# Optimization experiments

Hardware: AMD Instinct MI355X
Metric: run time of the kernel (lower is better)

Reference implementation:

```python
import jax, jax.numpy as jnp
import numpy as np
from jax.scipy.special import logsumexp

B, N, T, D = 32, 400, 315, 512   # batch, fMRI parcels, text/task rows, feature dim
H = 256
EPS = 1e-5                       # InstanceNorm2d default eps
N_ITERS = 100                    # sinkhorn_rpm n_iters


def setup_inputs() -> dict:
    key = jax.random.key(0)
    ks = jax.random.split(key, 6)
    features = jax.random.normal(ks[0], (B, N, D), jnp.float32)
    text = jax.random.normal(ks[1], (T, D), jnp.float32)
    # Affinity bilinear weight, init near identity as in graph-matching Affinity modules
    A = jnp.eye(D, dtype=jnp.float32) + 0.01 * jax.random.normal(ks[2], (D, D), jnp.float32)
    gamma = jnp.ones((), jnp.float32)   # InstanceNorm2d(1, affine=True) weight
    beta = jnp.zeros((), jnp.float32)   # InstanceNorm2d(1, affine=True) bias
    Wh = jax.random.normal(ks[3], (2 * D, H), jnp.float32) / np.float32(np.sqrt(2 * D))
    bh = jnp.zeros((H,), jnp.float32)
    Wo = jax.random.normal(ks[4], (H, 1), jnp.float32) / np.float32(np.sqrt(H))
    bo = jnp.zeros((1,), jnp.float32)
    return {"features": features, "text": text, "A": A, "gamma": gamma,
            "beta": beta, "Wh": Wh, "bh": bh, "Wo": Wo, "bo": bo}


def _forward(features, text, A, gamma, beta, Wh, bh, Wo, bo):
    # Affinity: s[b,n,t] = features[b,n,:] @ A @ text[t,:]   -> [B, N, T]
    s = jnp.einsum('bnd,de,te->bnt', features, A, text)
    # InstanceNorm2d(1, affine): normalize each [N,T] map per batch element (single channel)
    m = jnp.mean(s, axis=(1, 2), keepdims=True)
    v = jnp.var(s, axis=(1, 2), keepdims=True)
    s = gamma * (s - m) * jax.lax.rsqrt(v + EPS) + beta
    # sinkhorn_rpm: log-domain alternating row/col normalization, no slack
    def body(log_a, _):
        log_a = log_a - logsumexp(log_a, axis=2, keepdims=True)  # row normalization
        log_a = log_a - logsumexp(log_a, axis=1, keepdims=True)  # col normalization
        return log_a, None
    log_s, _ = jax.lax.scan(body, s, None, length=N_ITERS)
    s1 = jnp.exp(log_s)                                   # [B, N, T]
    # features_t @ s1, then transpose -> [B, T, D]
    features1 = jnp.einsum('bnd,bnt->btd', features, s1)
    text1 = jnp.broadcast_to(text[None], (features.shape[0], T, D))
    combine = jnp.concatenate([features1, text1], axis=2)  # [B, T, 2D]
    h = jax.nn.relu(combine @ Wh + bh)                     # [B, T, H]
    pred = (h @ Wo + bo)[..., 0]                           # [B, T] == [B, num_tasks]
    return pred


def reference(features, text, A, gamma, beta, Wh, bh, Wo, bo):
    return _forward(features, text, A, gamma, beta, Wh, bh, Wo, bo)
```

## Files before the change

kernel.cpp:

```cpp
#include <hip/hip_runtime.h>
#include <hip/hip_fp16.h>

#define BDIM 32
#define NDIM 400
#define TDIM 315
#define TPAD 320
#define DDIM 512
#define HDIM 256
#define NITER 100

#define OFS_TAB   0u
#define OFS_TB    327680u
#define OFS_STATS 655360u
#define OFS_WHB   655616u
#define OFS_S     1048576u
#define OFS_S1B   9240576u
#define OFS_F1    17432576u
#define OFS_FB    27754496u
#define OFS_QPART (OFS_F1 + 4096u)

typedef __attribute__((ext_vector_type(8))) short bf16x8;
typedef __attribute__((ext_vector_type(4))) float f32x4;
typedef unsigned long long ull;

__device__ __forceinline__ unsigned rne_hi(float x) {
  unsigned u = __float_as_uint(x);
  u += 0x7fffu + ((u >> 16) & 1u);
  return u & 0xffff0000u;
}
__device__ __forceinline__ unsigned pack2(float lo, float hi) {
  return (rne_hi(lo) >> 16) | rne_hi(hi);
}
__device__ __forceinline__ unsigned short bf1(float x) { return (unsigned short)(rne_hi(x) >> 16); }
__device__ __forceinline__ float bfres(float x) {
  return x - __uint_as_float(rne_hi(x));
}

template <int CTRL, int RMASK>
__device__ __forceinline__ float dppadd(float x) {
  int y = __builtin_amdgcn_update_dpp(0, __float_as_int(x), CTRL, RMASK, 0xf, true);
  return x + __int_as_float(y);
}
template <int CTRL, int RMASK>
__device__ __forceinline__ float dppmax(float x) {
  int y = __builtin_amdgcn_update_dpp(0, __float_as_int(x), CTRL, RMASK, 0xf, true);
  return fmaxf(x, __int_as_float(y));
}

#define LDH 40

__global__ __launch_bounds__(256) void k_prep(const float* __restrict__ F,
                                              const float* __restrict__ Wh,
                                              const float* __restrict__ text,
                                              const float* __restrict__ A,
                                              const float* __restrict__ bh,
                                              unsigned short* __restrict__ Fb,
                                              unsigned short* __restrict__ Whb,
                                              unsigned short* __restrict__ tAb,
                                              float* __restrict__ TB,
                                              float* __restrict__ stats,
                                              uint4* __restrict__ qzero) {
  __shared__ unsigned short Ahs[64 * LDH], Als[64 * LDH];
  __shared__ unsigned short Bhs[64 * LDH], Bls[64 * LDH];
  const int bid = blockIdx.x, tid = threadIdx.x;
  if (bid >= 60) {
    const int NF4 = (BDIM * NDIM * DDIM) / 4;
    const int NW4 = (DDIM * HDIM) / 4;
    const int NQ4 = (2 * BDIM * 8 * 320 * 2) / 4;
    const int gid = (bid - 60) * 256 + tid;
    const int stride = 452 * 256;
    for (int i = gid; i < NF4; i += stride) {
      float4 v = ((const float4*)F)[i];
      ((uint2*)Fb)[i] = make_uint2(pack2(v.x, v.y), pack2(v.z, v.w));
    }
    for (int i = gid; i < NW4; i += stride) {
      float4 v = ((const float4*)Wh)[i];
      ((uint2*)Whb)[i] = make_uint2(pack2(v.x, v.y), pack2(v.z, v.w));
    }
    for (int i = gid; i < NQ4; i += stride) qzero[i] = make_uint4(0u, 0u, 0u, 0u);
    if (gid < BDIM * 2) stats[gid] = 0.0f;
    return;
  }
  const int l = tid & 63, wv = tid >> 6;
  const int m = tid >> 2, kq = (tid & 3) * 8;
  f32x4 acc[4] = {};
  if (bid < 40) {
    const int d0 = (bid & 7) * 64, t0 = (bid >> 3) * 64;
    for (int k0 = 0; k0 < 512; k0 += 32) {
      {
        int t = t0 + m;
        float4 v0 = make_float4(0.f, 0.f, 0.f, 0.f), v1 = v0;
        if (t < TDIM) {
          v0 = *(const float4*)(text + (size_t)t * DDIM + k0 + kq);
          v1 = *(const float4*)(text + (size_t)t * DDIM + k0 + kq + 4);
        }
        *(uint4*)(&Ahs[m * LDH + kq]) =
            make_uint4(pack2(v0.x, v0.y), pack2(v0.z, v0.w), pack2(v1.x, v1.y), pack2(v1.z, v1.w));
        *(uint4*)(&Als[m * LDH + kq]) =
            make_uint4(pack2(bfres(v0.x), bfres(v0.y)), pack2(bfres(v0.z), bfres(v0.w)),
                       pack2(bfres(v1.x), bfres(v1.y)), pack2(bfres(v1.z), bfres(v1.w)));
        float4 w0 = *(const float4*)(A + (size_t)(d0 + m) * DDIM + k0 + kq);
        float4 w1 = *(const float4*)(A + (size_t)(d0 + m) * DDIM + k0 + kq + 4);
        *(uint4*)(&Bhs[m * LDH + kq]) =
            make_uint4(pack2(w0.x, w0.y), pack2(w0.z, w0.w), pack2(w1.x, w1.y), pack2(w1.z, w1.w));
        *(uint4*)(&Bls[m * LDH + kq]) =
            make_uint4(pack2(bfres(w0.x), bfres(w0.y)), pack2(bfres(w0.z), bfres(w0.w)),
                       pack2(bfres(w1.x), bfres(w1.y)), pack2(bfres(w1.z), bfres(w1.w)));
      }
      __syncthreads();
      bf16x8 ah = *(const bf16x8*)(&Ahs[(wv * 16 + (l & 15)) * LDH + (l >> 4) * 8]);
      bf16x8 al = *(const bf16x8*)(&Als[(wv * 16 + (l & 15)) * LDH + (l >> 4) * 8]);
#pragma unroll
      for (int c = 0; c < 4; ++c) {
        bf16x8 bh_ = *(const bf16x8*)(&Bhs[(c * 16 + (l & 15)) * LDH + (l >> 4) * 8]);
        bf16x8 bl_ = *(const bf16x8*)(&Bls[(c * 16 + (l & 15)) * LDH + (l >> 4) * 8]);
        acc[c] = __builtin_amdgcn_mfma_f32_16x16x32_bf16(ah, bh_, acc[c], 0, 0, 0);
        acc[c] = __builtin_amdgcn_mfma_f32_16x16x32_bf16(ah, bl_, acc[c], 0, 0, 0);
        acc[c] = __builtin_amdgcn_mfma_f32_16x16x32_bf16(al, bh_, acc[c], 0, 0, 0);
      }
      __syncthreads();
    }
#pragma unroll
    for (int c = 0; c < 4; ++c)
#pragma unroll
      for (int r = 0; r < 4; ++r) {
        int t = t0 + wv * 16 + ((l >> 4) << 2) + r;
        int d = d0 + c * 16 + (l & 15);
        tAb[(size_t)t * DDIM + d] = bf1(acc[c][r]);
      }
  } else {
    const int idx = bid - 40;
    const int h0 = (idx & 3) * 64, t0 = (idx >> 2) * 64;
    const float* Wb = Wh + DDIM * HDIM;
    const int col = tid & 31, g = tid >> 5;
    for (int k0 = 0; k0 < 512; k0 += 32) {
      {
        int t = t0 + m;
        float4 v0 = make_float4(0.f, 0.f, 0.f, 0.f), v1 = v0;
        if (t < TDIM) {
          v0 = *(const float4*)(text + (size_t)t * DDIM + k0 + kq);
          v1 = *(const float4*)(text + (size_t)t * DDIM + k0 + kq + 4);
        }
        *(uint4*)(&Ahs[m * LDH + kq]) =
            make_uint4(pack2(v0.x, v0.y), pack2(v0.z, v0.w), pack2(v1.x, v1.y), pack2(v1.z, v1.w));
        *(uint4*)(&Als[m * LDH + kq]) =
            make_uint4(pack2(bfres(v0.x), bfres(v0.y)), pack2(bfres(v0.z), bfres(v0.w)),
                       pack2(bfres(v1.x), bfres(v1.y)), pack2(bfres(v1.z), bfres(v1.w)));
        float4 w0 = *(const float4*)(Wb + (size_t)(k0 + col) * HDIM + h0 + g * 8);
        float4 w1 = *(const float4*)(Wb + (size_t)(k0 + col) * HDIM + h0 + g * 8 + 4);
        float wr[8] = {w0.x, w0.y, w0.z, w0.w, w1.x, w1.y, w1.z, w1.w};
#pragma unroll
        for (int i = 0; i < 8; ++i) {
          Bhs[(g * 8 + i) * LDH + col] = bf1(wr[i]);
          Bls[(g * 8 + i) * LDH + col] = bf1(bfres(wr[i]));
        }
      }
      __syncthreads();
      bf16x8 ah = *(const bf16x8*)(&Ahs[(wv * 16 + (l & 15)) * LDH + (l >> 4) * 8]);
      bf16x8 al = *(const bf16x8*)(&Als[(wv * 16 + (l & 15)) * LDH + (l >> 4) * 8]);
#pragma unroll
      for (int c = 0; c < 4; ++c) {
        bf16x8 bh_ = *(const bf16x8*)(&Bhs[(c * 16 + (l & 15)) * LDH + (l >> 4) * 8]);
        bf16x8 bl_ = *(const bf16x8*)(&Bls[(c * 16 + (l & 15)) * LDH + (l >> 4) * 8]);
        acc[c] = __builtin_amdgcn_mfma_f32_16x16x32_bf16(ah, bh_, acc[c], 0, 0, 0);
        acc[c] = __builtin_amdgcn_mfma_f32_16x16x32_bf16(ah, bl_, acc[c], 0, 0, 0);
        acc[c] = __builtin_amdgcn_mfma_f32_16x16x32_bf16(al, bh_, acc[c], 0, 0, 0);
      }
      __syncthreads();
    }
#pragma unroll
    for (int c = 0; c < 4; ++c)
#pragma unroll
      for (int r = 0; r < 4; ++r) {
        int t = t0 + wv * 16 + ((l >> 4) << 2) + r;
        int h = h0 + c * 16 + (l & 15);
        TB[(size_t)t * HDIM + h] = acc[c][r] + bh[h];
      }
  }
}

__global__ __launch_bounds__(256) void k_s(const unsigned short* __restrict__ Fb,
                                           const unsigned short* __restrict__ tAb,
                                           __half* __restrict__ s, float* __restrict__ stats) {
  __shared__ unsigned short Abf[64 * LDH];
  __shared__ unsigned short Bbf[64 * LDH];
  __shared__ float red[8];
  const int tid = threadIdx.x, l = tid & 63, wv = tid >> 6;
  const int bz = blockIdx.x, t0 = blockIdx.y * 64, n0 = blockIdx.z * 64;
  const unsigned short* Fbb = Fb + (size_t)bz * NDIM * DDIM;
  __half* sb = s + (size_t)bz * NDIM * TPAD;
  f32x4 acc[4] = {};
  const int m = tid >> 2, kq = (tid & 3) * 8;
  for (int k0 = 0; k0 < 512; k0 += 32) {
    uint4 av = make_uint4(0, 0, 0, 0);
    int n = n0 + m;
    if (n < NDIM) av = *(const uint4*)(Fbb + (size_t)n * DDIM + k0 + kq);
    *(uint4*)(&Abf[m * LDH + kq]) = av;
    uint4 bv = *(const uint4*)(tAb + (size_t)(t0 + m) * DDIM + k0 + kq);
    *(uint4*)(&Bbf[m * LDH + kq]) = bv;
    __syncthreads();
    bf16x8 af = *(const bf16x8*)(&Abf[(wv * 16 + (l & 15)) * LDH + (l >> 4) * 8]);
#pragma unroll
    for (int c = 0; c < 4; ++c) {
      bf16x8 bf_ = *(const bf16x8*)(&Bbf[(c * 16 + (l & 15)) * LDH + (l >> 4) * 8]);
      acc[c] = __builtin_amdgcn_mfma_f32_16x16x32_bf16(af, bf_, acc[c], 0, 0, 0);
    }
    __syncthreads();
  }
  float lsum = 0.f, lsq = 0.f;
#pragma unroll
  for (int c = 0; c < 4; ++c)
#pragma unroll
    for (int r = 0; r < 4; ++r) {
      int n = n0 + wv * 16 + ((l >> 4) << 2) + r;
      int t = t0 + c * 16 + (l & 15);
      if (n < NDIM && t < TDIM) {
        float v = acc[c][r];
        sb[(size_t)n * TPAD + t] = __float2half(v);
        lsum += v;
        lsq = fmaf(v, v, lsq);
      }
    }
#pragma unroll
  for (int mm = 1; mm <= 32; mm <<= 1) {
    lsum += __shfl_xor(lsum, mm, 64);
    lsq += __shfl_xor(lsq, mm, 64);
  }
  if ((tid & 63) == 0) { red[wv * 2] = lsum; red[wv * 2 + 1] = lsq; }
  __syncthreads();
  if (tid == 0) {
    float S = red[0] + red[2] + red[4] + red[6];
    float Q = red[1] + red[3] + red[5] + red[7];
    atomicAdd(&stats[bz * 2], S);
    atomicAdd(&stats[bz * 2 + 1], Q);
  }
}

#define SBLK 8
#define SROWS 50
#define SRPW 10

__global__ __launch_bounds__(320, 1) void k_sinkhorn(const __half* __restrict__ sbuf,
                                                     const float* __restrict__ stats,
                                                     const float* __restrict__ gptr,
                                                     const float* __restrict__ bptr,
                                                     unsigned short* __restrict__ s1b,
                                                     ull* __restrict__ qpart) {
  __shared__ float qpl[5][320];
  __shared__ float qg[5][320];
  const int b = blockIdx.x, c = blockIdx.y;
  const int tid = threadIdx.x, wv = tid >> 6, l = tid & 63;
  const __half* S = sbuf + (size_t)b * NDIM * TPAD;
  unsigned short* S1 = s1b + (size_t)b * NDIM * TPAD;
  const float NT = 400.0f * 315.0f;
  const float mean = stats[2 * b] / NT;
  const float var = stats[2 * b + 1] / NT - mean * mean;
  const float inv = rsqrtf(var + 1e-5f);
  const float alpha = gptr[0] * inv;
  const float L2E = 1.4426950408889634f;
  const float a2 = alpha * L2E;
  const float d2 = (bptr[0] - mean * alpha) * L2E;
  const int r0 = c * SROWS + wv * SRPW;
  const float TOL = 1e-3f;
  const float TN_RATIO = 315.0f / 400.0f;

  float E0[SRPW], E1[SRPW], E2[SRPW], E3[SRPW], E4[SRPW];
#pragma unroll
  for (int j = 0; j < SRPW; ++j) {
    const __half* row = S + (size_t)(r0 + j) * TPAD;
    E0[j] = __builtin_amdgcn_exp2f(fmaf(__half2float(row[l]), a2, d2));
    E1[j] = __builtin_amdgcn_exp2f(fmaf(__half2float(row[64 + l]), a2, d2));
    E2[j] = __builtin_amdgcn_exp2f(fmaf(__half2float(row[128 + l]), a2, d2));
    E3[j] = __builtin_amdgcn_exp2f(fmaf(__half2float(row[192 + l]), a2, d2));
    E4[j] = (l < 59) ? __builtin_amdgcn_exp2f(fmaf(__half2float(row[256 + l]), a2, d2)) : 0.0f;
  }
  float w0 = 1.0f, w1 = 1.0f, w2 = 1.0f, w3 = 1.0f, w4 = (l < 59) ? 1.0f : 0.0f;
  float aj[SRPW];
#pragma unroll
  for (int j = 0; j < SRPW; ++j) aj[j] = 0.0f;

  bool fin = false;
  for (int it = 0; it < NITER; ++it) {
    float p[SRPW];
#pragma unroll
    for (int j = 0; j < SRPW; ++j) {
      float t = E4[j] * w4;
      t = fmaf(E3[j], w3, t);
      t = fmaf(E2[j], w2, t);
      t = fmaf(E1[j], w1, t);
      p[j] = fmaf(E0[j], w0, t);
    }
#pragma unroll
    for (int j = 0; j < SRPW; ++j) p[j] = dppadd<0x111, 0xf>(p[j]);
#pragma unroll
    for (int j = 0; j < SRPW; ++j) p[j] = dppadd<0x112, 0xf>(p[j]);
#pragma unroll
    for (int j = 0; j < SRPW; ++j) p[j] = dppadd<0x114, 0xf>(p[j]);
#pragma unroll
    for (int j = 0; j < SRPW; ++j) p[j] = dppadd<0x118, 0xf>(p[j]);
#pragma unroll
    for (int j = 0; j < SRPW; ++j) p[j] = dppadd<0x142, 0xa>(p[j]);
#pragma unroll
    for (int j = 0; j < SRPW; ++j) p[j] = dppadd<0x143, 0xc>(p[j]);
#pragma unroll
    for (int j = 0; j < SRPW; ++j) {
      float r = __builtin_amdgcn_rcpf(p[j]);
      aj[j] = __int_as_float(__builtin_amdgcn_readlane(__float_as_int(r), 63));
    }
    float q0 = 0.f, q1 = 0.f, q2 = 0.f, q3 = 0.f, q4 = 0.f;
#pragma unroll
    for (int j = 0; j < SRPW; ++j) {
      q0 = fmaf(E0[j], aj[j], q0);
      q1 = fmaf(E1[j], aj[j], q1);
      q2 = fmaf(E2[j], aj[j], q2);
      q3 = fmaf(E3[j], aj[j], q3);
      q4 = fmaf(E4[j], aj[j], q4);
    }
    qpl[wv][l] = q0;
    qpl[wv][64 + l] = q1;
    qpl[wv][128 + l] = q2;
    qpl[wv][192 + l] = q3;
    qpl[wv][256 + l] = q4;
    __syncthreads();
    const int par = it & 1;
    const unsigned tgt = (unsigned)(it + 1);
    ull* bufpar = qpart + ((size_t)par * BDIM + b) * (SBLK * 320);
    if (wv == 0) {
      ull* myp = bufpar + c * 320;
#pragma unroll
      for (int k = 0; k < 5; ++k) {
        int t = k * 64 + l;
        float sm = qpl[0][t] + qpl[1][t] + qpl[2][t] + qpl[3][t] + qpl[4][t];
        __hip_atomic_store(&myp[t], ((ull)tgt << 32) | (ull)__float_as_uint(sm),
                           __ATOMIC_RELAXED, __HIP_MEMORY_SCOPE_AGENT);
      }
    }
    {
      const int ncc = (wv < 3) ? 2 : 1;
      ull got[2][5];
      const int ccs[2] = {wv, wv + 5};
#pragma unroll
      for (int e = 0; e < 2; ++e)
        if (e < ncc && ccs[e] != c) {
#pragma unroll
          for (int k = 0; k < 5; ++k)
            got[e][k] = __hip_atomic_load(&bufpar[ccs[e] * 320 + k * 64 + l],
                                          __ATOMIC_RELAXED, __HIP_MEMORY_SCOPE_AGENT);
        }
      int guard = 0;
      for (;;) {
        bool ok = true;
#pragma unroll
        for (int e = 0; e < 2; ++e)
          if (e < ncc && ccs[e] != c) {
#pragma unroll
            for (int k = 0; k < 5; ++k)
              if ((unsigned)(got[e][k] >> 32) != tgt) {
                got[e][k] = __hip_atomic_load(&bufpar[ccs[e] * 320 + k * 64 + l],
                                              __ATOMIC_RELAXED, __HIP_MEMORY_SCOPE_AGENT);
                ok = false;
              }
          }
        if (ok) break;
        if (++guard > (1 << 20)) break;
      }
      float part[5] = {0.f, 0.f, 0.f, 0.f, 0.f};
#pragma unroll
      for (int e = 0; e < 2; ++e)
        if (e < ncc) {
#pragma unroll
          for (int k = 0; k < 5; ++k) {
            int t = k * 64 + l;
            float v = (ccs[e] == c)
                          ? (qpl[0][t] + qpl[1][t] + qpl[2][t] + qpl[3][t] + qpl[4][t])
                          : __uint_as_float((unsigned)got[e][k]);
            part[k] += v;
          }
        }
#pragma unroll
      for (int k = 0; k < 5; ++k) qg[wv][k * 64 + l] = part[k];
    }
    __syncthreads();
    const float Q0 = qg[0][l] + qg[1][l] + qg[2][l] + qg[3][l] + qg[4][l];
    const float Q1 = qg[0][64 + l] + qg[1][64 + l] + qg[2][64 + l] + qg[3][64 + l] + qg[4][64 + l];
    const float Q2 =
        qg[0][128 + l] + qg[1][128 + l] + qg[2][128 + l] + qg[3][128 + l] + qg[4][128 + l];
    const float Q3 =
        qg[0][192 + l] + qg[1][192 + l] + qg[2][192 + l] + qg[3][192 + l] + qg[4][192 + l];
    const float Q4 =
        qg[0][256 + l] + qg[1][256 + l] + qg[2][256 + l] + qg[3][256 + l] + qg[4][256 + l];
    float r = fabsf(fmaf(Q0 * w0, TN_RATIO, -1.0f));
    r = fmaxf(r, fabsf(fmaf(Q1 * w1, TN_RATIO, -1.0f)));
    r = fmaxf(r, fabsf(fmaf(Q2 * w2, TN_RATIO, -1.0f)));
    r = fmaxf(r, fabsf(fmaf(Q3 * w3, TN_RATIO, -1.0f)));
    if (l < 59) r = fmaxf(r, fabsf(fmaf(Q4 * w4, TN_RATIO, -1.0f)));
    w0 = __builtin_amdgcn_rcpf(Q0);
    w1 = __builtin_amdgcn_rcpf(Q1);
    w2 = __builtin_amdgcn_rcpf(Q2);
    w3 = __builtin_amdgcn_rcpf(Q3);
    if (l < 59) w4 = __builtin_amdgcn_rcpf(Q4);
    if (fin) break;
    r = dppmax<0x111, 0xf>(r);
    r = dppmax<0x112, 0xf>(r);
    r = dppmax<0x114, 0xf>(r);
    r = dppmax<0x118, 0xf>(r);
    r = dppmax<0x142, 0xa>(r);
    r = dppmax<0x143, 0xc>(r);
    const float resid = __int_as_float(__builtin_amdgcn_readlane(__float_as_int(r), 63));
    fin = (resid < TOL) || (it == NITER - 2);
  }

#pragma unroll
  for (int j = 0; j < SRPW; ++j) {
    unsigned short* row = S1 + (size_t)(r0 + j) * TPAD;
    const float a = aj[j];
    row[l] = bf1(a * E0[j] * w0);
    row[64 + l] = bf1(a * E1[j] * w1);
    row[128 + l] = bf1(a * E2[j] * w2);
    row[192 + l] = bf1(a * E3[j] * w3);
    row[256 + l] = (l < 59) ? bf1(a * E4[j] * w4) : (unsigned short)0;
  }
}

__global__ __launch_bounds__(256) void k_f1(const unsigned short* __restrict__ s1b,
                                            const unsigned short* __restrict__ Fb,
                                            unsigned short* __restrict__ f1b) {
  __shared__ unsigned short Abf[64 * LDH];
  __shared__ unsigned short Bbf[64 * LDH];
  const int tid = threadIdx.x, l = tid & 63, wv = tid >> 6;
  const int bz = blockIdx.x, d0 = blockIdx.y * 64, t0 = blockIdx.z * 64;
  const unsigned short* sb = s1b + (size_t)bz * NDIM * TPAD;
  const unsigned short* Fbb = Fb + (size_t)bz * NDIM * DDIM;
  unsigned short* out = f1b + (size_t)bz * TDIM * DDIM;
  f32x4 acc[4] = {};
  const int col = tid & 31, g = tid >> 5;
  for (int k0 = 0; k0 < 416; k0 += 32) {
    int n = k0 + col;
    uint4 av = make_uint4(0, 0, 0, 0), bv = av;
    if (n < NDIM) {
      av = *(const uint4*)(sb + (size_t)n * TPAD + t0 + g * 8);
      bv = *(const uint4*)(Fbb + (size_t)n * DDIM + d0 + g * 8);
    }
    unsigned short ah[8], bh8[8];
    *(uint4*)ah = av;
    *(uint4*)bh8 = bv;
#pragma unroll
    for (int i = 0; i < 8; ++i) {
      Abf[(g * 8 + i) * LDH + col] = ah[i];
      Bbf[(g * 8 + i) * LDH + col] = bh8[i];
    }
    __syncthreads();
    bf16x8 af = *(const bf16x8*)(&Abf[(wv * 16 + (l & 15)) * LDH + (l >> 4) * 8]);
#pragma unroll
    for (int c = 0; c < 4; ++c) {
      bf16x8 bf_ = *(const bf16x8*)(&Bbf[(c * 16 + (l & 15)) * LDH + (l >> 4) * 8]);
      acc[c] = __builtin_amdgcn_mfma_f32_16x16x32_bf16(af, bf_, acc[c], 0, 0, 0);
    }
    __syncthreads();
  }
#pragma unroll
  for (int c = 0; c < 4; ++c)
#pragma unroll
    for (int r = 0; r < 4; ++r) {
      int t = t0 + wv * 16 + ((l >> 4) << 2) + r;
      int d = d0 + c * 16 + (l & 15);
      if (t < TDIM) out[(size_t)t * DDIM + d] = bf1(acc[c][r]);
    }
}

__global__ __launch_bounds__(256) void k_hp(const unsigned short* __restrict__ f1b,
                                            const unsigned short* __restrict__ Whb,
                                            const float* __restrict__ TB,
                                            const float* __restrict__ Wo,
                                            const float* __restrict__ bo,
                                            float* __restrict__ out) {
  __shared__ unsigned short Abf[64 * LDH];
  __shared__ unsigned short Bbf[256 * LDH];
  __shared__ float Wos[256];
  const int tid = threadIdx.x, l = tid & 63, wv = tid >> 6;
  const int r0 = blockIdx.x * 64;
  const int RTOT = BDIM * TDIM;
  Wos[tid] = Wo[tid];
  f32x4 acc[16] = {};
  const int m = tid >> 2, kq = (tid & 3) * 8;
  const int col = tid & 31, g = tid >> 5;
  for (int k0 = 0; k0 < 512; k0 += 32) {
    uint4 av = make_uint4(0, 0, 0, 0);
    int r = r0 + m;
    if (r < RTOT) av = *(const uint4*)(f1b + (size_t)r * DDIM + k0 + kq);
    *(uint4*)(&Abf[m * LDH + kq]) = av;
#pragma unroll
    for (int p = 0; p < 4; ++p) {
      uint4 bv = *(const uint4*)(Whb + (size_t)(k0 + col) * HDIM + p * 64 + g * 8);
      unsigned short bh8[8];
      *(uint4*)bh8 = bv;
#pragma unroll
      for (int i = 0; i < 8; ++i) Bbf[(p * 64 + g * 8 + i) * LDH + col] = bh8[i];
    }
    __syncthreads();
    bf16x8 af = *(const bf16x8*)(&Abf[(wv * 16 + (l & 15)) * LDH + (l >> 4) * 8]);
#pragma unroll
    for (int c = 0; c < 16; ++c) {
      bf16x8 bf_ = *(const bf16x8*)(&Bbf[(c * 16 + (l & 15)) * LDH + (l >> 4) * 8]);
      acc[c] = __builtin_amdgcn_mfma_f32_16x16x32_bf16(af, bf_, acc[c], 0, 0, 0);
    }
    __syncthreads();
  }
  int tmod[4];
#pragma unroll
  for (int r = 0; r < 4; ++r) {
    int rr = r0 + wv * 16 + ((l >> 4) << 2) + r;
    tmod[r] = rr % TDIM;
  }
  float part[4] = {0.f, 0.f, 0.f, 0.f};
#pragma unroll
  for (int c = 0; c < 16; ++c) {
    int jl = c * 16 + (l & 15);
    float woc = Wos[jl];
#pragma unroll
    for (int r = 0; r < 4; ++r) {
      float v = acc[c][r] + TB[(size_t)tmod[r] * HDIM + jl];
      part[r] = fmaf(fmaxf(v, 0.f), woc, part[r]);
    }
  }
#pragma unroll
  for (int r = 0; r < 4; ++r) part[r] = dppadd<0x111, 0xf>(part[r]);
#pragma unroll
  for (int r = 0; r < 4; ++r) part[r] = dppadd<0x112, 0xf>(part[r]);
#pragma unroll
  for (int r = 0; r < 4; ++r) part[r] = dppadd<0x114, 0xf>(part[r]);
#pragma unroll
  for (int r = 0; r < 4; ++r) part[r] = dppadd<0x118, 0xf>(part[r]);
  if ((l & 15) == 15) {
    const float base = bo[0];
#pragma unroll
    for (int r = 0; r < 4; ++r) {
      int rr = r0 + wv * 16 + ((l >> 4) << 2) + r;
      if (rr < RTOT) out[rr] = part[r] + base;
    }
  }
}

extern "C" void kernel_launch(void* const* d_in, const int* in_sizes, int n_in,
                              void* d_out, int out_size, void* d_ws, size_t ws_size,
                              hipStream_t stream) {
  const float* F     = (const float*)d_in[0];
  const float* text  = (const float*)d_in[1];
  const float* A     = (const float*)d_in[2];
  const float* gamma = (const float*)d_in[3];
  const float* beta  = (const float*)d_in[4];
  const float* Wh    = (const float*)d_in[5];
  const float* bh    = (const float*)d_in[6];
  const float* Wo    = (const float*)d_in[7];
  const float* bo    = (const float*)d_in[8];
  float* out = (float*)d_out;
  char* ws = (char*)d_ws;
  unsigned short* tAb = (unsigned short*)(ws + OFS_TAB);
  float* TB    = (float*)(ws + OFS_TB);
  float* stats = (float*)(ws + OFS_STATS);
  unsigned short* Whb = (unsigned short*)(ws + OFS_WHB);
  __half* sbuf = (__half*)(ws + OFS_S);
  unsigned short* s1b = (unsigned short*)(ws + OFS_S1B);
  unsigned short* f1b = (unsigned short*)(ws + OFS_F1);
  unsigned short* Fb  = (unsigned short*)(ws + OFS_FB);
  ull* qpart = (ull*)(ws + OFS_QPART);

  k_prep<<<512, 256, 0, stream>>>(F, Wh, text, A, bh, Fb, Whb, tAb, TB, stats, (uint4*)qpart);
  k_s<<<dim3(32, 5, 7), 256, 0, stream>>>(Fb, tAb, sbuf, stats);
  k_sinkhorn<<<dim3(BDIM, SBLK), 320, 0, stream>>>(sbuf, stats, gamma, beta, s1b, qpart);
  k_f1<<<dim3(32, 8, 5), 256, 0, stream>>>(s1b, Fb, f1b);
  k_hp<<<dim3(158), 256, 0, stream>>>(f1b, Whb, TB, Wo, bo, out);
}
```

Before: 196.3 us.

## Fuse affinity GEMM and instance-norm stats into the sinkhorn kernel

Removes the separate k_s kernel. Each sinkhorn block now computes its own 50x320 slice of the affinity map with MFMA into shared memory. The per-batch mean and variance come from partial sums that the 8 blocks of a batch publish and then spin-wait on through global atomics. This drops the fp16 s buffer round trip through HBM and one launch, but puts a GEMM inside a 1-block-per-CU kernel with only 256 blocks, and relies on every block of a batch being co-resident for the spin barrier.

```diff
diff --git a/kernel.cpp b/kernel.cpp
--- a/kernel.cpp
+++ b/kernel.cpp
@@ -11,13 +11,12 @@
 
 #define OFS_TAB   0u
 #define OFS_TB    327680u
-#define OFS_STATS 655360u
 #define OFS_WHB   655616u
-#define OFS_S     1048576u
 #define OFS_S1B   9240576u
 #define OFS_F1    17432576u
 #define OFS_FB    27754496u
 #define OFS_QPART (OFS_F1 + 4096u)
+#define QSTATS    163840u
 
 typedef __attribute__((ext_vector_type(8))) short bf16x8;
 typedef __attribute__((ext_vector_type(4))) float f32x4;
@@ -58,7 +57,6 @@
                                               unsigned short* __restrict__ Whb,
                                               unsigned short* __restrict__ tAb,
                                               float* __restrict__ TB,
-                                              float* __restrict__ stats,
                                               uint4* __restrict__ qzero) {
   __shared__ unsigned short Ahs[64 * LDH], Als[64 * LDH];
   __shared__ unsigned short Bhs[64 * LDH], Bls[64 * LDH];
@@ -66,7 +64,7 @@
   if (bid >= 60) {
     const int NF4 = (BDIM * NDIM * DDIM) / 4;
     const int NW4 = (DDIM * HDIM) / 4;
-    const int NQ4 = (2 * BDIM * 8 * 320 * 2) / 4;
+    const int NQ4 = (2 * BDIM * 8 * 320 * 2 + BDIM * 8 * 2 * 2) / 4;
     const int gid = (bid - 60) * 256 + tid;
     const int stride = 452 * 256;
     for (int i = gid; i < NF4; i += stride) {
@@ -78,7 +76,6 @@
       ((uint2*)Whb)[i] = make_uint2(pack2(v.x, v.y), pack2(v.z, v.w));
     }
     for (int i = gid; i < NQ4; i += stride) qzero[i] = make_uint4(0u, 0u, 0u, 0u);
-    if (gid < BDIM * 2) stats[gid] = 0.0f;
     return;
   }
   const int l = tid & 63, wv = tid >> 6;
@@ -179,100 +176,135 @@
   }
 }
 
-__global__ __launch_bounds__(256) void k_s(const unsigned short* __restrict__ Fb,
-                                           const unsigned short* __restrict__ tAb,
-                                           __half* __restrict__ s, float* __restrict__ stats) {
-  __shared__ unsigned short Abf[64 * LDH];
-  __shared__ unsigned short Bbf[64 * LDH];
-  __shared__ float red[8];
-  const int tid = threadIdx.x, l = tid & 63, wv = tid >> 6;
-  const int bz = blockIdx.x, t0 = blockIdx.y * 64, n0 = blockIdx.z * 64;
-  const unsigned short* Fbb = Fb + (size_t)bz * NDIM * DDIM;
-  __half* sb = s + (size_t)bz * NDIM * TPAD;
-  f32x4 acc[4] = {};
-  const int m = tid >> 2, kq = (tid & 3) * 8;
-  for (int k0 = 0; k0 < 512; k0 += 32) {
-    uint4 av = make_uint4(0, 0, 0, 0);
-    int n = n0 + m;
-    if (n < NDIM) av = *(const uint4*)(Fbb + (size_t)n * DDIM + k0 + kq);
-    *(uint4*)(&Abf[m * LDH + kq]) = av;
-    uint4 bv = *(const uint4*)(tAb + (size_t)(t0 + m) * DDIM + k0 + kq);
-    *(uint4*)(&Bbf[m * LDH + kq]) = bv;
-    __syncthreads();
-    bf16x8 af = *(const bf16x8*)(&Abf[(wv * 16 + (l & 15)) * LDH + (l >> 4) * 8]);
-#pragma unroll
-    for (int c = 0; c < 4; ++c) {
-      bf16x8 bf_ = *(const bf16x8*)(&Bbf[(c * 16 + (l & 15)) * LDH + (l >> 4) * 8]);
-      acc[c] = __builtin_amdgcn_mfma_f32_16x16x32_bf16(af, bf_, acc[c], 0, 0, 0);
-    }
-    __syncthreads();
-  }
-  float lsum = 0.f, lsq = 0.f;
-#pragma unroll
-  for (int c = 0; c < 4; ++c)
-#pragma unroll
-    for (int r = 0; r < 4; ++r) {
-      int n = n0 + wv * 16 + ((l >> 4) << 2) + r;
-      int t = t0 + c * 16 + (l & 15);
-      if (n < NDIM && t < TDIM) {
-        float v = acc[c][r];
-        sb[(size_t)n * TPAD + t] = __float2half(v);
-        lsum += v;
-        lsq = fmaf(v, v, lsq);
-      }
-    }
-#pragma unroll
-  for (int mm = 1; mm <= 32; mm <<= 1) {
-    lsum += __shfl_xor(lsum, mm, 64);
-    lsq += __shfl_xor(lsq, mm, 64);
-  }
-  if ((tid & 63) == 0) { red[wv * 2] = lsum; red[wv * 2 + 1] = lsq; }
-  __syncthreads();
-  if (tid == 0) {
-    float S = red[0] + red[2] + red[4] + red[6];
-    float Q = red[1] + red[3] + red[5] + red[7];
-    atomicAdd(&stats[bz * 2], S);
-    atomicAdd(&stats[bz * 2 + 1], Q);
-  }
-}
-
 #define SBLK 8
 #define SROWS 50
 #define SRPW 10
 
-__global__ __launch_bounds__(320, 1) void k_sinkhorn(const __half* __restrict__ sbuf,
-                                                     const float* __restrict__ stats,
+__global__ __launch_bounds__(320, 1) void k_sinkhorn(const unsigned short* __restrict__ Fb,
+                                                     const unsigned short* __restrict__ tAb,
                                                      const float* __restrict__ gptr,
                                                      const float* __restrict__ bptr,
                                                      unsigned short* __restrict__ s1b,
                                                      ull* __restrict__ qpart) {
+  __shared__ unsigned short Fch[64 * LDH];
+  __shared__ unsigned short tACh[320 * LDH];
+  __shared__ float Sls[SROWS * 320];
   __shared__ float qpl[5][320];
   __shared__ float qg[5][320];
+  __shared__ float sred[16];
   const int b = blockIdx.x, c = blockIdx.y;
   const int tid = threadIdx.x, wv = tid >> 6, l = tid & 63;
-  const __half* S = sbuf + (size_t)b * NDIM * TPAD;
   unsigned short* S1 = s1b + (size_t)b * NDIM * TPAD;
+  const unsigned short* Fbb = Fb + (size_t)b * NDIM * DDIM + (size_t)c * SROWS * DDIM;
+  const float TOL = 1e-3f;
+  const float TN_RATIO = 315.0f / 400.0f;
+
+  f32x4 acc[16] = {};
+  {
+    const int m = tid >> 2, kq = (tid & 3) * 8;
+    for (int k0 = 0; k0 < 512; k0 += 32) {
+      if (m < 64) {
+        uint4 fv = make_uint4(0, 0, 0, 0);
+        if (m < SROWS) fv = *(const uint4*)(Fbb + (size_t)m * DDIM + k0 + kq);
+        *(uint4*)(&Fch[m * LDH + kq]) = fv;
+      }
+#pragma unroll
+      for (int p = 0; p < 4; ++p) {
+        int row = p * 80 + m;
+        *(uint4*)(&tACh[row * LDH + kq]) = *(const uint4*)(tAb + (size_t)row * DDIM + k0 + kq);
+      }
+      __syncthreads();
+      bf16x8 af[4];
+#pragma unroll
+      for (int nt = 0; nt < 4; ++nt)
+        af[nt] = *(const bf16x8*)(&Fch[(nt * 16 + (l & 15)) * LDH + (l >> 4) * 8]);
+#pragma unroll
+      for (int tt = 0; tt < 4; ++tt) {
+        bf16x8 bf_ = *(const bf16x8*)(&tACh[((wv * 4 + tt) * 16 + (l & 15)) * LDH + (l >> 4) * 8]);
+#pragma unroll
+        for (int nt = 0; nt < 4; ++nt)
+          acc[tt * 4 + nt] = __builtin_amdgcn_mfma_f32_16x16x32_bf16(af[nt], bf_, acc[tt * 4 + nt], 0, 0, 0);
+      }
+      __syncthreads();
+    }
+  }
+  float ls = 0.f, lq = 0.f;
+#pragma unroll
+  for (int tt = 0; tt < 4; ++tt) {
+    int t = (wv * 4 + tt) * 16 + (l & 15);
+    bool tv = (t < TDIM);
+#pragma unroll
+    for (int nt = 0; nt < 4; ++nt)
+#pragma unroll
+      for (int r = 0; r < 4; ++r) {
+        int n = nt * 16 + ((l >> 4) << 2) + r;
+        if (n < SROWS && tv) {
+          float v = acc[tt * 4 + nt][r];
+          Sls[n * 320 + t] = v;
+          ls += v;
+          lq = fmaf(v, v, lq);
+        }
+      }
+  }
+#pragma unroll
+  for (int mm = 1; mm <= 32; mm <<= 1) {
+    ls += __shfl_xor(ls, mm, 64);
+    lq += __shfl_xor(lq, mm, 64);
+  }
+  if (l == 0) { sred[wv] = ls; sred[8 + wv] = lq; }
+  __syncthreads();
+  {
+    ull* satoms = qpart + QSTATS;
+    if (tid == 0) {
+      float Ssum = sred[0] + sred[1] + sred[2] + sred[3] + sred[4];
+      float Sq = sred[8] + sred[9] + sred[10] + sred[11] + sred[12];
+      ull* mine = satoms + ((size_t)b * SBLK + c) * 2;
+      __hip_atomic_store(&mine[0], (1ull << 32) | (ull)__float_as_uint(Ssum),
+                         __ATOMIC_RELAXED, __HIP_MEMORY_SCOPE_AGENT);
+      __hip_atomic_store(&mine[1], (1ull << 32) | (ull)__float_as_uint(Sq),
+                         __ATOMIC_RELAXED, __HIP_MEMORY_SCOPE_AGENT);
+    }
+    if (wv == 0) {
+      ull g = (1ull << 32);
+      const ull* base = satoms + (size_t)b * SBLK * 2;
+      if (l < 16) g = __hip_atomic_load(&base[l], __ATOMIC_RELAXED, __HIP_MEMORY_SCOPE_AGENT);
+      int guard = 0;
+      while (!((unsigned)(g >> 32) >= 1u)) {
+        if (++guard > (1 << 20)) break;
+        if (l < 16) g = __hip_atomic_load(&base[l], __ATOMIC_RELAXED, __HIP_MEMORY_SCOPE_AGENT);
+      }
+      for (;;) {
+        if (__ballot((unsigned)(g >> 32) >= 1u) == ~0ull) break;
+        if (l < 16 && (unsigned)(g >> 32) < 1u)
+          g = __hip_atomic_load(&base[l], __ATOMIC_RELAXED, __HIP_MEMORY_SCOPE_AGENT);
+      }
+      if (l < 16) sred[l] = __uint_as_float((unsigned)g);
+    }
+  }
+  __syncthreads();
   const float NT = 400.0f * 315.0f;
-  const float mean = stats[2 * b] / NT;
-  const float var = stats[2 * b + 1] / NT - mean * mean;
+  const float Ssum_all = ((sred[0] + sred[2]) + (sred[4] + sred[6])) +
+                         ((sred[8] + sred[10]) + (sred[12] + sred[14]));
+  const float Sq_all = ((sred[1] + sred[3]) + (sred[5] + sred[7])) +
+                       ((sred[9] + sred[11]) + (sred[13] + sred[15]));
+  const float mean = Ssum_all / NT;
+  const float var = Sq_all / NT - mean * mean;
   const float inv = rsqrtf(var + 1e-5f);
   const float alpha = gptr[0] * inv;
   const float L2E = 1.4426950408889634f;
   const float a2 = alpha * L2E;
   const float d2 = (bptr[0] - mean * alpha) * L2E;
   const int r0 = c * SROWS + wv * SRPW;
-  const float TOL = 1e-3f;
-  const float TN_RATIO = 315.0f / 400.0f;
 
   float E0[SRPW], E1[SRPW], E2[SRPW], E3[SRPW], E4[SRPW];
 #pragma unroll
   for (int j = 0; j < SRPW; ++j) {
-    const __half* row = S + (size_t)(r0 + j) * TPAD;
-    E0[j] = __builtin_amdgcn_exp2f(fmaf(__half2float(row[l]), a2, d2));
-    E1[j] = __builtin_amdgcn_exp2f(fmaf(__half2float(row[64 + l]), a2, d2));
-    E2[j] = __builtin_amdgcn_exp2f(fmaf(__half2float(row[128 + l]), a2, d2));
-    E3[j] = __builtin_amdgcn_exp2f(fmaf(__half2float(row[192 + l]), a2, d2));
-    E4[j] = (l < 59) ? __builtin_amdgcn_exp2f(fmaf(__half2float(row[256 + l]), a2, d2)) : 0.0f;
+    const float* row = Sls + (wv * SRPW + j) * 320;
+    E0[j] = __builtin_amdgcn_exp2f(fmaf(row[l], a2, d2));
+    E1[j] = __builtin_amdgcn_exp2f(fmaf(row[64 + l], a2, d2));
+    E2[j] = __builtin_amdgcn_exp2f(fmaf(row[128 + l], a2, d2));
+    E3[j] = __builtin_amdgcn_exp2f(fmaf(row[192 + l], a2, d2));
+    E4[j] = (l < 59) ? __builtin_amdgcn_exp2f(fmaf(row[256 + l], a2, d2)) : 0.0f;
   }
   float w0 = 1.0f, w1 = 1.0f, w2 = 1.0f, w3 = 1.0f, w4 = (l < 59) ? 1.0f : 0.0f;
   float aj[SRPW];
@@ -557,17 +589,14 @@
   char* ws = (char*)d_ws;
   unsigned short* tAb = (unsigned short*)(ws + OFS_TAB);
   float* TB    = (float*)(ws + OFS_TB);
-  float* stats = (float*)(ws + OFS_STATS);
   unsigned short* Whb = (unsigned short*)(ws + OFS_WHB);
-  __half* sbuf = (__half*)(ws + OFS_S);
   unsigned short* s1b = (unsigned short*)(ws + OFS_S1B);
   unsigned short* f1b = (unsigned short*)(ws + OFS_F1);
   unsigned short* Fb  = (unsigned short*)(ws + OFS_FB);
   ull* qpart = (ull*)(ws + OFS_QPART);
 
-  k_prep<<<512, 256, 0, stream>>>(F, Wh, text, A, bh, Fb, Whb, tAb, TB, stats, (uint4*)qpart);
-  k_s<<<dim3(32, 5, 7), 256, 0, stream>>>(Fb, tAb, sbuf, stats);
-  k_sinkhorn<<<dim3(BDIM, SBLK), 320, 0, stream>>>(sbuf, stats, gamma, beta, s1b, qpart);
+  k_prep<<<512, 256, 0, stream>>>(F, Wh, text, A, bh, Fb, Whb, tAb, TB, (uint4*)qpart);
+  k_sinkhorn<<<dim3(BDIM, SBLK), 320, 0, stream>>>(Fb, tAb, gamma, beta, s1b, qpart);
   k_f1<<<dim3(32, 8, 5), 256, 0, stream>>>(s1b, Fb, f1b);
   k_hp<<<dim3(158), 256, 0, stream>>>(f1b, Whb, TB, Wo, bo, out);
 }
```

Measured after the change: 185.8 us. 1.06x faster.
